# Kernel tuning notes

Hardware: AMD Instinct MI355X
Metric: run time of the kernel (lower is better)

The kernel has to match this reference:

```python
import jax, jax.numpy as jnp
import numpy as np

NUM_BRANCHES = 3
NUM_LAYERS = 4
HIDDEN = 256
IN_DIM = 128
NUM_GRAPHS = 256
NUM_CLASSES = 10
TOPK_RATIO = 0.5
GATE_INIT = 0.8


def matrix_neighbors(branch, layer, num_branches):
    nbrs = []
    if layer > 0:
        nbrs.append((branch, layer - 1))
    for other in (branch - 1, branch + 1):
        if 0 <= other < num_branches:
            nbrs.append((other, layer))
    if layer > 0:
        for other in (branch - 1, branch + 1):
            if 0 <= other < num_branches:
                nbrs.append((other, layer - 1))
    return nbrs


def topk_mask(t, ratio):
    d = t.shape[-1]
    k = max(1, min(d, int(np.ceil(d * ratio))))
    if k >= d:
        return jnp.ones_like(t)
    _, idx = jax.lax.top_k(jnp.abs(t), k)
    rows = jnp.arange(t.shape[0])[:, None]
    return jnp.zeros_like(t).at[rows, idx].set(1.0)


def setup_inputs():
    key = jax.random.key(0)
    ks = jax.random.split(key, 10)
    n, e = 50000, 800000
    x = jax.random.normal(ks[0], (n, IN_DIM), dtype=jnp.float32)
    edge_index = jax.random.randint(ks[1], (2, e), 0, n)
    batch = jnp.sort(jax.random.randint(ks[2], (n,), 0, NUM_GRAPHS))
    s = 0.05
    Win = jax.random.normal(ks[3], (NUM_BRANCHES, IN_DIM, HIDDEN), dtype=jnp.float32) * s
    b_in = jnp.zeros((NUM_BRANCHES, HIDDEN), dtype=jnp.float32)
    Whid = jax.random.normal(ks[4], (NUM_LAYERS - 1, NUM_BRANCHES, HIDDEN, HIDDEN), dtype=jnp.float32) * s
    bhid = jnp.zeros((NUM_LAYERS - 1, NUM_BRANCHES, HIDDEN), dtype=jnp.float32)
    gate_logit = jnp.asarray(np.log(GATE_INIT / (1.0 - GATE_INIT)), dtype=jnp.float32)
    Wc = jax.random.normal(ks[5], (HIDDEN, NUM_CLASSES), dtype=jnp.float32) * s
    bc = jnp.zeros((NUM_CLASSES,), dtype=jnp.float32)
    return {"x": x, "edge_index": edge_index, "batch": batch, "Win": Win,
            "b_in": b_in, "Whid": Whid, "bhid": bhid, "gate_logit": gate_logit,
            "Wc": Wc, "bc": bc}


def _forward(x, edge_index, batch, Win, b_in, Whid, bhid, gate_logit, Wc, bc):
    n = x.shape[0]
    loops = jnp.arange(n)
    row = jnp.concatenate([edge_index[0], loops])  # source
    col = jnp.concatenate([edge_index[1], loops])  # target
    deg = jax.ops.segment_sum(jnp.ones_like(col, dtype=x.dtype), col, num_segments=n)
    dinv = jnp.where(deg > 0, jax.lax.rsqrt(deg), 0.0)
    norm = dinv[row] * dinv[col]  # [E+N]

    def gcn(h, W, b):
        hw = h @ W  # [n, H]
        agg = jax.ops.segment_sum(hw[row] * norm[:, None], col, num_segments=n)
        return agg + b

    gate = jax.nn.sigmoid(gate_logit)
    states = [x for _ in range(NUM_BRANCHES)]
    for layer in range(NUM_LAYERS):
        props = []
        for b in range(NUM_BRANCHES):
            if layer == 0:
                p = gcn(states[b], Win[b], b_in[b])
            else:
                p = gcn(states[b], Whid[layer - 1, b], bhid[layer - 1, b])
            props.append(jax.nn.relu(p))
        new_states = []
        for b in range(NUM_BRANCHES):
            fused = props[b]
            nbrs = matrix_neighbors(b, layer, NUM_BRANCHES)
            if nbrs:
                rs = jnp.zeros_like(fused)
                for (sb, sl) in nbrs:
                    src = props[sb] if sl == layer else states[sb]
                    rs = rs + src * topk_mask(src, TOPK_RATIO)
                fused = fused + gate * rs
            new_states.append(jax.nn.relu(fused))  # dropout is identity in eval
        states = new_states

    counts = jax.ops.segment_sum(jnp.ones((n,), dtype=x.dtype), batch, num_segments=NUM_GRAPHS)
    denom = jnp.maximum(counts, 1.0)[:, None]
    embs = [jax.ops.segment_sum(s, batch, num_segments=NUM_GRAPHS) / denom for s in states]
    final = jnp.mean(jnp.stack(embs, axis=0), axis=0)  # [G, H]
    logits = final @ Wc + bc
    return logits, final


def reference(x, edge_index, batch, Win, b_in, Whid, bhid, gate_logit, Wc, bc):
    return _forward(x, edge_index, batch, Win, b_in, Whid, bhid, gate_logit, Wc, bc)
```

## Files before the change

kernel.cpp:

```cpp
#include <hip/hip_runtime.h>
#include <hip/hip_fp16.h>

#define NB 3
#define HIDDEN 256
#define INDIM 128
#define NGRAPH 256
#define NCLS 10
#define NMAX 50048
#define EMAX 800000

typedef unsigned short u16;
typedef unsigned long long ull;
typedef _Float16 f16_t;
typedef f16_t f16x8 __attribute__((ext_vector_type(8)));
typedef float f32x4 __attribute__((ext_vector_type(4)));

__device__ __align__(16) u16   g_states[(size_t)NMAX * NB * HIDDEN];
__device__ __align__(16) u16   g_props [(size_t)NMAX * NB * HIDDEN];
__device__ __align__(16) u16   g_agg3 [(size_t)NMAX * NB * HIDDEN];
__device__ __align__(16) u16   g_xh    [(size_t)NMAX * INDIM];
__device__ __align__(16) u16   g_whin [(size_t)NB * INDIM * HIDDEN];
__device__ __align__(16) u16   g_whid [(size_t)9 * HIDDEN * HIDDEN];
__device__ float g_fin   [NGRAPH * HIDDEN];
__device__ float g_dinv  [NMAX];
__device__ float g_ewts  [EMAX];
__device__ int   g_rowptr[NMAX + 1];
__device__ int   g_cidx  [EMAX];
__device__ int   g_cnt   [NMAX];
__device__ int   g_bsum  [64];
__device__ int   g_gs    [NGRAPH];
__device__ int   g_gc    [NGRAPH];

union HU { u16 u; __half h; };
__device__ __forceinline__ float h2f(u16 v) { HU x; x.u = v; return __half2float(x.h); }
__device__ __forceinline__ u16 f2h(float f) { HU x; x.h = __float2half_rn(f); return x.u; }
__device__ __forceinline__ float relu_f(float x) { return x > 0.f ? x : 0.f; }

__device__ __forceinline__ void fma8(float* acc, uint4 v, float w) {
    unsigned uu[4] = {v.x, v.y, v.z, v.w};
    #pragma unroll
    for (int q = 0; q < 4; ++q) {
        HU lo, hi; lo.u = (u16)(uu[q] & 0xFFFFu); hi.u = (u16)(uu[q] >> 16);
        acc[q * 2 + 0] += w * __half2float(lo.h);
        acc[q * 2 + 1] += w * __half2float(hi.h);
    }
}

__global__ void zero_cnt_k(int n) {
    int i = blockIdx.x * 256 + threadIdx.x;
    if (i < n) g_cnt[i] = 0;
}
__global__ void zero_gk() {
    int i = threadIdx.x;
    g_gs[i] = 0; g_gc[i] = 0;
}
__global__ void cvt_xh_k(const float* __restrict__ x, int cnt4) {
    int i = blockIdx.x * 256 + threadIdx.x;
    if (i >= cnt4) return;
    float4 v = ((const float4*)x)[i];
    ushort4 o; o.x = f2h(v.x); o.y = f2h(v.y); o.z = f2h(v.z); o.w = f2h(v.w);
    ((ushort4*)g_xh)[i] = o;
}
__global__ void cvt_wt_k(const float* __restrict__ src, int which, int K) {
    __shared__ u16 tile[32][33];
    int k0 = blockIdx.x * 32, c0 = blockIdx.y * 32, b = blockIdx.z;
    int t = threadIdx.x;
    int tc = t & 31, tk = t >> 5;
    const float* S = src + (size_t)b * K * 256;
    #pragma unroll
    for (int q = 0; q < 4; ++q) {
        int kk = tk * 4 + q;
        tile[kk][tc] = f2h(S[(size_t)(k0 + kk) * 256 + c0 + tc]);
    }
    __syncthreads();
    u16* D = (which ? g_whid : g_whin) + (size_t)b * K * 256;
    int kx = t & 31, cg = t >> 5;
    #pragma unroll
    for (int q = 0; q < 4; ++q) {
        int c = c0 + cg * 4 + q;
        D[(size_t)c * K + k0 + kx] = tile[kx][cg * 4 + q];
    }
}

__global__ void count_edges_k(const int* __restrict__ col, int E) {
    int i = blockIdx.x * 256 + threadIdx.x;
    if (i < E) atomicAdd(&g_cnt[col[i]], 1);
}
__global__ void dinv_k(int n) {
    int i = blockIdx.x * 256 + threadIdx.x;
    if (i < n) g_dinv[i] = rsqrtf((float)(g_cnt[i] + 1));
}
__global__ __launch_bounds__(1024) void scan1_k(int n) {
    __shared__ int sm[1024];
    int blk = blockIdx.x, t = threadIdx.x;
    int i = blk * 1024 + t;
    int v = (i < n) ? g_cnt[i] : 0;
    sm[t] = v;
    __syncthreads();
    for (int off = 1; off < 1024; off <<= 1) {
        int u = (t >= off) ? sm[t - off] : 0;
        __syncthreads();
        sm[t] += u;
        __syncthreads();
    }
    if (i < n) g_rowptr[i + 1] = sm[t];
    if (t == 1023) g_bsum[blk] = sm[t];
    if (blk == 0 && t == 0) g_rowptr[0] = 0;
}
__global__ void scan2_k(int nblk) {
    int t = threadIdx.x;
    int v = (t < nblk) ? g_bsum[t] : 0;
    #pragma unroll
    for (int off = 1; off < 64; off <<= 1) {
        int u = __shfl_up(v, off);
        if (t >= off) v += u;
    }
    if (t < nblk) g_bsum[t] = v;
}
__global__ void scan3_k(int n) {
    int i = blockIdx.x * 256 + threadIdx.x;
    if (i >= n) return;
    int blk = i >> 10;
    if (blk > 0) g_rowptr[i + 1] += g_bsum[blk - 1];
}
__global__ void fill_csr_k(const int* __restrict__ row, const int* __restrict__ col, int E) {
    int i = blockIdx.x * 256 + threadIdx.x;
    if (i >= E) return;
    int r = row[i], c = col[i];
    int pos = g_rowptr[c] + atomicAdd(&g_cnt[c], 1);
    g_cidx[pos] = r;
    g_ewts[pos] = g_dinv[r] * g_dinv[c];
}

__global__ __launch_bounds__(256) void agg256x3_k(int n) {
    int node = blockIdx.x * 4 + (threadIdx.x >> 6);
    if (node >= n) return;
    int lane = threadIdx.x & 63;
    int half = lane >> 5;
    int li   = lane & 31;
    const uint4* Sv = (const uint4*)g_states;
    float acc0[8] = {0,0,0,0,0,0,0,0}, acc1[8] = {0,0,0,0,0,0,0,0}, acc2[8] = {0,0,0,0,0,0,0,0};
    int e0 = g_rowptr[node], deg = g_rowptr[node + 1] - e0;
    int m = deg + 1;
    int j = half;
    if (half == 0) {
        float di = g_dinv[node];
        float w0 = di * di;
        size_t base = (size_t)node * 96 + li;
        fma8(acc0, Sv[base], w0);
        fma8(acc1, Sv[base + 32], w0);
        fma8(acc2, Sv[base + 64], w0);
        j = 2;
    }
    #pragma unroll 2
    for (; j < m; j += 2) {
        int s = g_cidx[e0 + j - 1];
        float w = g_ewts[e0 + j - 1];
        size_t base = (size_t)s * 96 + li;
        uint4 v0 = Sv[base], v1 = Sv[base + 32], v2 = Sv[base + 64];
        fma8(acc0, v0, w); fma8(acc1, v1, w); fma8(acc2, v2, w);
    }
    #pragma unroll
    for (int q = 0; q < 8; ++q) {
        acc0[q] += __shfl_xor(acc0[q], 32);
        acc1[q] += __shfl_xor(acc1[q], 32);
        acc2[q] += __shfl_xor(acc2[q], 32);
    }
    if (half == 0) {
        uint4* Av = (uint4*)g_agg3;
        size_t base = (size_t)node * 96 + li;
        uint4 o;
        unsigned* ou = (unsigned*)&o;
        #pragma unroll
        for (int q = 0; q < 4; ++q) ou[q] = (unsigned)f2h(acc0[q*2]) | ((unsigned)f2h(acc0[q*2+1]) << 16);
        Av[base] = o;
        #pragma unroll
        for (int q = 0; q < 4; ++q) ou[q] = (unsigned)f2h(acc1[q*2]) | ((unsigned)f2h(acc1[q*2+1]) << 16);
        Av[base + 32] = o;
        #pragma unroll
        for (int q = 0; q < 4; ++q) ou[q] = (unsigned)f2h(acc2[q*2]) | ((unsigned)f2h(acc2[q*2+1]) << 16);
        Av[base + 64] = o;
    }
}

__global__ __launch_bounds__(256) void agg128_k(int n) {
    int node = blockIdx.x * 4 + (threadIdx.x >> 6);
    if (node >= n) return;
    int lane = threadIdx.x & 63;
    int grp = lane >> 4;
    int li  = lane & 15;
    const uint4* Xv = (const uint4*)g_xh;
    float acc[8] = {0,0,0,0,0,0,0,0};
    int e0 = g_rowptr[node], deg = g_rowptr[node + 1] - e0;
    int m = deg + 1;
    int j = grp;
    if (grp == 0) {
        float di = g_dinv[node];
        fma8(acc, Xv[(size_t)node * 16 + li], di * di);
        j = 4;
    }
    #pragma unroll 2
    for (; j < m; j += 4) {
        int s = g_cidx[e0 + j - 1];
        float w = g_ewts[e0 + j - 1];
        fma8(acc, Xv[(size_t)s * 16 + li], w);
    }
    #pragma unroll
    for (int q = 0; q < 8; ++q) {
        acc[q] += __shfl_xor(acc[q], 16);
        acc[q] += __shfl_xor(acc[q], 32);
    }
    if (grp == 0) {
        uint4 o; unsigned* ou = (unsigned*)&o;
        #pragma unroll
        for (int q = 0; q < 4; ++q) ou[q] = (unsigned)f2h(acc[q*2]) | ((unsigned)f2h(acc[q*2+1]) << 16);
        ((uint4*)g_agg3)[(size_t)node * 16 + li] = o;
    }
}

template<int K>
__global__ __launch_bounds__(256) void gemm_mfma_k(int wsel, int rowStride, int brMul,
        const float* __restrict__ bias0, int n) {
    int br = blockIdx.y;
    const f16_t* A  = (const f16_t*)g_agg3 + (size_t)br * brMul;
    const f16_t* Wt = (wsel < 0) ? (const f16_t*)g_whin + (size_t)br * K * 256
                                 : (const f16_t*)g_whid + (size_t)(wsel + br) * K * 256;
    const float* bias = bias0 + (size_t)br * 256;
    u16* C = g_props + (size_t)br * 256;
    int t = threadIdx.x, l = t & 63, w = t >> 6;
    int row0 = blockIdx.x * 64;
    int c0 = w * 64;
    int mrow = l & 15;
    int kg = (l >> 4) * 8;
    f32x4 acc[4][4];
    #pragma unroll
    for (int rt = 0; rt < 4; ++rt)
        #pragma unroll
        for (int ct = 0; ct < 4; ++ct) acc[rt][ct] = (f32x4){0.f, 0.f, 0.f, 0.f};

    for (int k0 = 0; k0 < K; k0 += 32) {
        f16x8 af[4], bf[4];
        #pragma unroll
        for (int rt = 0; rt < 4; ++rt) {
            int r = row0 + rt * 16 + mrow;
            af[rt] = *(const f16x8*)(A + (size_t)r * rowStride + k0 + kg);
        }
        #pragma unroll
        for (int ct = 0; ct < 4; ++ct) {
            int c = c0 + ct * 16 + mrow;
            bf[ct] = *(const f16x8*)(Wt + (size_t)c * K + k0 + kg);
        }
        #pragma unroll
        for (int rt = 0; rt < 4; ++rt)
            #pragma unroll
            for (int ct = 0; ct < 4; ++ct)
                acc[rt][ct] = __builtin_amdgcn_mfma_f32_16x16x32_f16(af[rt], bf[ct], acc[rt][ct], 0, 0, 0);
    }
    int rb = (l >> 4) * 4;
    #pragma unroll
    for (int ct = 0; ct < 4; ++ct) {
        int c = c0 + ct * 16 + mrow;
        float bv = bias[c];
        #pragma unroll
        for (int rt = 0; rt < 4; ++rt) {
            #pragma unroll
            for (int q = 0; q < 4; ++q) {
                int r = row0 + rt * 16 + rb + q;
                if (r < n) C[(size_t)r * 768 + c] = f2h(relu_f(acc[rt][ct][q] + bv));
            }
        }
    }
}

template<int CNT>
__device__ __forceinline__ void topk_multi(const ushort4* hu, const float4* v, float4* out) {
    int lane = threadIdx.x & 63;
    unsigned lo[CNT], hi[CNT]; int cge[CNT];
    #pragma unroll
    for (int s = 0; s < CNT; ++s) {
        unsigned mx = max(max((unsigned)hu[s].x, (unsigned)hu[s].y),
                          max((unsigned)hu[s].z, (unsigned)hu[s].w));
        #pragma unroll
        for (int off = 32; off >= 1; off >>= 1)
            mx = max(mx, (unsigned)__shfl_xor((int)mx, off));
        lo[s] = 0; hi[s] = mx; cge[s] = 256;
    }
    for (int it = 0; it < 15; ++it) {
        #pragma unroll
        for (int s = 0; s < CNT; ++s) {
            if (cge[s] == 128 || lo[s] >= hi[s]) continue;
            unsigned mid = (lo[s] + hi[s] + 1) >> 1;
            int c = __popcll(__ballot(hu[s].x >= mid)) + __popcll(__ballot(hu[s].y >= mid))
                  + __popcll(__ballot(hu[s].z >= mid)) + __popcll(__ballot(hu[s].w >= mid));
            if (c >= 128) { lo[s] = mid; cge[s] = c; } else hi[s] = mid - 1;
        }
    }
    #pragma unroll
    for (int s = 0; s < CNT; ++s) {
        unsigned thr = lo[s];
        unsigned a0 = hu[s].x, a1 = hu[s].y, a2 = hu[s].z, a3 = hu[s].w;
        float4 r;
        if (cge[s] == 128) {
            r.x = (a0 >= thr) ? v[s].x : 0.f;
            r.y = (a1 >= thr) ? v[s].y : 0.f;
            r.z = (a2 >= thr) ? v[s].z : 0.f;
            r.w = (a3 >= thr) ? v[s].w : 0.f;
        } else {
            ull b0 = __ballot(a0 == thr), b1 = __ballot(a1 == thr);
            ull b2 = __ballot(a2 == thr), b3 = __ballot(a3 == thr);
            int cgt = __popcll(__ballot(a0 > thr)) + __popcll(__ballot(a1 > thr))
                    + __popcll(__ballot(a2 > thr)) + __popcll(__ballot(a3 > thr));
            int need = 128 - cgt;
            ull below = (lane == 0) ? 0ull : (~0ull >> (64 - lane));
            int base = __popcll(b0 & below) + __popcll(b1 & below)
                     + __popcll(b2 & below) + __popcll(b3 & below);
            int o0 = (int)((b0 >> lane) & 1), o1 = (int)((b1 >> lane) & 1), o2 = (int)((b2 >> lane) & 1);
            int p0 = base, p1 = base + o0, p2 = p1 + o1, p3 = p2 + o2;
            r.x = (a0 > thr || (a0 == thr && p0 < need)) ? v[s].x : 0.f;
            r.y = (a1 > thr || (a1 == thr && p1 < need)) ? v[s].y : 0.f;
            r.z = (a2 > thr || (a2 == thr && p2 < need)) ? v[s].z : 0.f;
            r.w = (a3 > thr || (a3 == thr && p3 < need)) ? v[s].w : 0.f;
        }
        out[s] = r;
    }
}

__device__ __forceinline__ float4 dec4(ushort4 h) {
    float4 r; r.x = h2f(h.x); r.y = h2f(h.y); r.z = h2f(h.z); r.w = h2f(h.w);
    return r;
}
__device__ __forceinline__ void st4h(u16* p, size_t off, float4 v) {
    ushort4 o; o.x = f2h(v.x); o.y = f2h(v.y); o.z = f2h(v.z); o.w = f2h(v.w);
    ((ushort4*)p)[off] = o;
}

__global__ __launch_bounds__(256) void fuse0_k(const float* __restrict__ gate_logit, int n) {
    int node = blockIdx.x * 4 + (threadIdx.x >> 6);
    if (node >= n) return;
    int lane = threadIdx.x & 63;
    size_t base4 = (size_t)node * 192 + lane;
    float g = 1.f / (1.f + expf(-gate_logit[0]));
    const ushort4* P = (const ushort4*)g_props;
    ushort4 hu[3]; float4 v[3], m[3];
    hu[0] = P[base4]; hu[1] = P[base4 + 64]; hu[2] = P[base4 + 128];
    v[0] = dec4(hu[0]); v[1] = dec4(hu[1]); v[2] = dec4(hu[2]);
    topk_multi<3>(hu, v, m);
    float4 o0, o1, o2;
    o0.x = relu_f(v[0].x + g * m[1].x); o0.y = relu_f(v[0].y + g * m[1].y);
    o0.z = relu_f(v[0].z + g * m[1].z); o0.w = relu_f(v[0].w + g * m[1].w);
    o1.x = relu_f(v[1].x + g * (m[0].x + m[2].x)); o1.y = relu_f(v[1].y + g * (m[0].y + m[2].y));
    o1.z = relu_f(v[1].z + g * (m[0].z + m[2].z)); o1.w = relu_f(v[1].w + g * (m[0].w + m[2].w));
    o2.x = relu_f(v[2].x + g * m[1].x); o2.y = relu_f(v[2].y + g * m[1].y);
    o2.z = relu_f(v[2].z + g * m[1].z); o2.w = relu_f(v[2].w + g * m[1].w);
    st4h(g_states, base4, o0); st4h(g_states, base4 + 64, o1); st4h(g_states, base4 + 128, o2);
}

__global__ __launch_bounds__(256) void fuse_k(const float* __restrict__ gate_logit, int n) {
    int node = blockIdx.x * 4 + (threadIdx.x >> 6);
    if (node >= n) return;
    int lane = threadIdx.x & 63;
    size_t base4 = (size_t)node * 192 + lane;
    float g = 1.f / (1.f + expf(-gate_logit[0]));
    const ushort4* P = (const ushort4*)g_props;
    const ushort4* S = (const ushort4*)g_states;
    ushort4 hu[6]; float4 v[6], m[6];
    hu[0] = P[base4]; hu[1] = P[base4 + 64]; hu[2] = P[base4 + 128];
    hu[3] = S[base4]; hu[4] = S[base4 + 64]; hu[5] = S[base4 + 128];
    #pragma unroll
    for (int s = 0; s < 6; ++s) v[s] = dec4(hu[s]);
    topk_multi<6>(hu, v, m);
    float4 o0, o1, o2;
    o0.x = relu_f(v[0].x + g * (m[3].x + m[1].x + m[4].x));
    o0.y = relu_f(v[0].y + g * (m[3].y + m[1].y + m[4].y));
    o0.z = relu_f(v[0].z + g * (m[3].z + m[1].z + m[4].z));
    o0.w = relu_f(v[0].w + g * (m[3].w + m[1].w + m[4].w));
    o1.x = relu_f(v[1].x + g * (m[4].x + m[0].x + m[3].x + m[2].x + m[5].x));
    o1.y = relu_f(v[1].y + g * (m[4].y + m[0].y + m[3].y + m[2].y + m[5].y));
    o1.z = relu_f(v[1].z + g * (m[4].z + m[0].z + m[3].z + m[2].z + m[5].z));
    o1.w = relu_f(v[1].w + g * (m[4].w + m[0].w + m[3].w + m[2].w + m[5].w));
    o2.x = relu_f(v[2].x + g * (m[5].x + m[1].x + m[4].x));
    o2.y = relu_f(v[2].y + g * (m[5].y + m[1].y + m[4].y));
    o2.z = relu_f(v[2].z + g * (m[5].z + m[1].z + m[4].z));
    o2.w = relu_f(v[2].w + g * (m[5].w + m[1].w + m[4].w));
    st4h(g_states, base4, o0); st4h(g_states, base4 + 64, o1); st4h(g_states, base4 + 128, o2);
}

__global__ void gbounds_k(const int* __restrict__ batch, int n) {
    int i = blockIdx.x * 256 + threadIdx.x;
    if (i >= n) return;
    int g = batch[i];
    atomicAdd(&g_gc[g], 1);
    if (i == 0 || batch[i - 1] != g) g_gs[g] = i;
}

__global__ __launch_bounds__(256) void greduce_k(float* __restrict__ outfin, int n) {
    __shared__ float sums[768];
    int g = blockIdx.x, t = threadIdx.x;
    int st = g_gs[g], c = g_gc[g];
    if (t < 192) {
        const ushort4* S = (const ushort4*)g_states;
        float a0 = 0.f, a1 = 0.f, a2 = 0.f, a3 = 0.f;
        for (int i = st; i < st + c; ++i) {
            ushort4 v = S[(size_t)i * 192 + t];
            a0 += h2f(v.x); a1 += h2f(v.y); a2 += h2f(v.z); a3 += h2f(v.w);
        }
        sums[t * 4 + 0] = a0; sums[t * 4 + 1] = a1;
        sums[t * 4 + 2] = a2; sums[t * 4 + 3] = a3;
    }
    __syncthreads();
    float r = (sums[t] + sums[256 + t] + sums[512 + t]) / (3.0f * (float)(c > 0 ? c : 1));
    g_fin[g * 256 + t] = r;
    outfin[(size_t)g * 256 + t] = r;
}

__global__ void logits_k(const float* __restrict__ Wc, const float* __restrict__ bc,
                         float* __restrict__ out) {
    int idx = blockIdx.x * 256 + threadIdx.x;
    if (idx >= NGRAPH * NCLS) return;
    int g = idx / NCLS, c = idx % NCLS;
    float s = bc[c];
    for (int k = 0; k < 256; ++k) s += g_fin[g * 256 + k] * Wc[k * NCLS + c];
    out[idx] = s;
}

extern "C" void kernel_launch(void* const* d_in, const int* in_sizes, int n_in,
                              void* d_out, int out_size, void* d_ws, size_t ws_size,
                              hipStream_t stream) {
    const float* x       = (const float*)d_in[0];
    const int*   eidx    = (const int*)d_in[1];
    const int*   batch   = (const int*)d_in[2];
    const float* Win     = (const float*)d_in[3];
    const float* b_in    = (const float*)d_in[4];
    const float* Whid    = (const float*)d_in[5];
    const float* bhid    = (const float*)d_in[6];
    const float* gate_l  = (const float*)d_in[7];
    const float* Wc      = (const float*)d_in[8];
    const float* bc      = (const float*)d_in[9];
    float* out = (float*)d_out;

    const int n = in_sizes[0] / INDIM;
    const int E = in_sizes[1] / 2;
    if (n > NMAX || E > EMAX) return;
    const int* erow = eidx;
    const int* ecol = eidx + E;

    float* outfin = out + NGRAPH * NCLS;

    const int TB = 256;
    dim3 b256(TB);
    int nblkN = (n + TB - 1) / TB;
    int eblk  = (E + TB - 1) / TB;
    int nblk4 = (n + 3) / 4;
    int sblk  = (n + 1023) / 1024;
    dim3 ggrid((n + 63) / 64, NB);
    dim3 wgin(INDIM / 32, HIDDEN / 32, NB);
    dim3 wghid(HIDDEN / 32, HIDDEN / 32, 9);

    zero_cnt_k<<<nblkN, b256, 0, stream>>>(n);
    cvt_xh_k<<<(n * INDIM / 4 + TB - 1) / TB, b256, 0, stream>>>(x, n * INDIM / 4);
    cvt_wt_k<<<wgin, b256, 0, stream>>>(Win, 0, INDIM);
    cvt_wt_k<<<wghid, b256, 0, stream>>>(Whid, 1, HIDDEN);
    count_edges_k<<<eblk, b256, 0, stream>>>(ecol, E);
    dinv_k<<<nblkN, b256, 0, stream>>>(n);
    scan1_k<<<sblk, 1024, 0, stream>>>(n);
    scan2_k<<<1, 64, 0, stream>>>(sblk);
    scan3_k<<<nblkN, b256, 0, stream>>>(n);
    zero_cnt_k<<<nblkN, b256, 0, stream>>>(n);
    fill_csr_k<<<eblk, b256, 0, stream>>>(erow, ecol, E);

    agg128_k<<<nblk4, b256, 0, stream>>>(n);
    gemm_mfma_k<INDIM><<<ggrid, b256, 0, stream>>>(-1, INDIM, 0, b_in, n);
    fuse0_k<<<nblk4, b256, 0, stream>>>(gate_l, n);

    for (int l = 1; l < 4; ++l) {
        agg256x3_k<<<nblk4, b256, 0, stream>>>(n);
        gemm_mfma_k<HIDDEN><<<ggrid, b256, 0, stream>>>((l - 1) * NB, NB * HIDDEN, HIDDEN,
                bhid + (size_t)(l - 1) * NB * HIDDEN, n);
        fuse_k<<<nblk4, b256, 0, stream>>>(gate_l, n);
    }

    zero_gk<<<1, 256, 0, stream>>>();
    gbounds_k<<<nblkN, b256, 0, stream>>>(batch, n);
    greduce_k<<<NGRAPH, b256, 0, stream>>>(outfin, n);
    logits_k<<<(NGRAPH * NCLS + TB - 1) / TB, b256, 0, stream>>>(Wc, bc, out);
}
```

Measured before the change: 1.698 ms.

## Fuse per-layer GEMM with top-k gated fusion via shared-memory staging

Merges the MFMA GEMM and the top-k fuse kernel into one kernel. Each block computes all three branches for 32 nodes, stages the relu'd results in LDS, then runs the top-k mixing and writes the states directly. This removes the g_props global round trip and one launch per layer. In exchange the row tile is halved to 32, so weights are reloaded more often per output row, and the large LDS footprint may lower occupancy.

New measurement: 1.937 ms. +14.1%, slower.

```diff
diff --git a/kernel.cpp b/kernel.cpp
--- a/kernel.cpp
+++ b/kernel.cpp
@@ -16,7 +16,6 @@
 typedef float f32x4 __attribute__((ext_vector_type(4)));
 
 __device__ __align__(16) u16   g_states[(size_t)NMAX * NB * HIDDEN];
-__device__ __align__(16) u16   g_props [(size_t)NMAX * NB * HIDDEN];
 __device__ __align__(16) u16   g_agg3 [(size_t)NMAX * NB * HIDDEN];
 __device__ __align__(16) u16   g_xh    [(size_t)NMAX * INDIM];
 __device__ __align__(16) u16   g_whin [(size_t)NB * INDIM * HIDDEN];
@@ -215,60 +214,6 @@
         #pragma unroll
         for (int q = 0; q < 4; ++q) ou[q] = (unsigned)f2h(acc[q*2]) | ((unsigned)f2h(acc[q*2+1]) << 16);
         ((uint4*)g_agg3)[(size_t)node * 16 + li] = o;
-    }
-}
-
-template<int K>
-__global__ __launch_bounds__(256) void gemm_mfma_k(int wsel, int rowStride, int brMul,
-        const float* __restrict__ bias0, int n) {
-    int br = blockIdx.y;
-    const f16_t* A  = (const f16_t*)g_agg3 + (size_t)br * brMul;
-    const f16_t* Wt = (wsel < 0) ? (const f16_t*)g_whin + (size_t)br * K * 256
-                                 : (const f16_t*)g_whid + (size_t)(wsel + br) * K * 256;
-    const float* bias = bias0 + (size_t)br * 256;
-    u16* C = g_props + (size_t)br * 256;
-    int t = threadIdx.x, l = t & 63, w = t >> 6;
-    int row0 = blockIdx.x * 64;
-    int c0 = w * 64;
-    int mrow = l & 15;
-    int kg = (l >> 4) * 8;
-    f32x4 acc[4][4];
-    #pragma unroll
-    for (int rt = 0; rt < 4; ++rt)
-        #pragma unroll
-        for (int ct = 0; ct < 4; ++ct) acc[rt][ct] = (f32x4){0.f, 0.f, 0.f, 0.f};
-
-    for (int k0 = 0; k0 < K; k0 += 32) {
-        f16x8 af[4], bf[4];
-        #pragma unroll
-        for (int rt = 0; rt < 4; ++rt) {
-            int r = row0 + rt * 16 + mrow;
-            af[rt] = *(const f16x8*)(A + (size_t)r * rowStride + k0 + kg);
-        }
-        #pragma unroll
-        for (int ct = 0; ct < 4; ++ct) {
-            int c = c0 + ct * 16 + mrow;
-            bf[ct] = *(const f16x8*)(Wt + (size_t)c * K + k0 + kg);
-        }
-        #pragma unroll
-        for (int rt = 0; rt < 4; ++rt)
-            #pragma unroll
-            for (int ct = 0; ct < 4; ++ct)
-                acc[rt][ct] = __builtin_amdgcn_mfma_f32_16x16x32_f16(af[rt], bf[ct], acc[rt][ct], 0, 0, 0);
-    }
-    int rb = (l >> 4) * 4;
-    #pragma unroll
-    for (int ct = 0; ct < 4; ++ct) {
-        int c = c0 + ct * 16 + mrow;
-        float bv = bias[c];
-        #pragma unroll
-        for (int rt = 0; rt < 4; ++rt) {
-            #pragma unroll
-            for (int q = 0; q < 4; ++q) {
-                int r = row0 + rt * 16 + rb + q;
-                if (r < n) C[(size_t)r * 768 + c] = f2h(relu_f(acc[rt][ct][q] + bv));
-            }
-        }
     }
 }
 
@@ -334,55 +279,103 @@
     ((ushort4*)p)[off] = o;
 }
 
-__global__ __launch_bounds__(256) void fuse0_k(const float* __restrict__ gate_logit, int n) {
-    int node = blockIdx.x * 4 + (threadIdx.x >> 6);
-    if (node >= n) return;
-    int lane = threadIdx.x & 63;
-    size_t base4 = (size_t)node * 192 + lane;
+#define LDSW 776
+template<int K, bool L0>
+__global__ __launch_bounds__(256) void gemm_fuse_k(int wsel, int rowStride, int brMul,
+        const float* __restrict__ bias0, const float* __restrict__ gate_logit, int n) {
+    __shared__ u16 lds_p[32 * LDSW];
+    int t = threadIdx.x, l = t & 63, w = t >> 6;
+    int row0 = blockIdx.x * 32;
+    int mrow = l & 15;
+    int kg = (l >> 4) * 8;
+    int rb = (l >> 4) * 4;
+
+    for (int br = 0; br < NB; ++br) {
+        const f16_t* A  = (const f16_t*)g_agg3 + (size_t)br * brMul;
+        const f16_t* Wt = (wsel < 0) ? (const f16_t*)g_whin + (size_t)br * K * 256
+                                     : (const f16_t*)g_whid + (size_t)(wsel + br) * K * 256;
+        const float* bias = bias0 + (size_t)br * 256;
+        f32x4 acc[2][4];
+        #pragma unroll
+        for (int rt = 0; rt < 2; ++rt)
+            #pragma unroll
+            for (int ct = 0; ct < 4; ++ct) acc[rt][ct] = (f32x4){0.f, 0.f, 0.f, 0.f};
+        for (int k0 = 0; k0 < K; k0 += 32) {
+            f16x8 af[2], bf[4];
+            #pragma unroll
+            for (int rt = 0; rt < 2; ++rt) {
+                int r = row0 + rt * 16 + mrow;
+                af[rt] = *(const f16x8*)(A + (size_t)r * rowStride + k0 + kg);
+            }
+            #pragma unroll
+            for (int ct = 0; ct < 4; ++ct) {
+                int c = w * 64 + ct * 16 + mrow;
+                bf[ct] = *(const f16x8*)(Wt + (size_t)c * K + k0 + kg);
+            }
+            #pragma unroll
+            for (int rt = 0; rt < 2; ++rt)
+                #pragma unroll
+                for (int ct = 0; ct < 4; ++ct)
+                    acc[rt][ct] = __builtin_amdgcn_mfma_f32_16x16x32_f16(af[rt], bf[ct], acc[rt][ct], 0, 0, 0);
+        }
+        #pragma unroll
+        for (int ct = 0; ct < 4; ++ct) {
+            int c = w * 64 + ct * 16 + mrow;
+            float bv = bias[c];
+            #pragma unroll
+            for (int rt = 0; rt < 2; ++rt) {
+                #pragma unroll
+                for (int q = 0; q < 4; ++q) {
+                    int ndl = rt * 16 + rb + q;
+                    lds_p[ndl * LDSW + br * 256 + c] = f2h(relu_f(acc[rt][ct][q] + bv));
+                }
+            }
+        }
+    }
+    __syncthreads();
+
     float g = 1.f / (1.f + expf(-gate_logit[0]));
-    const ushort4* P = (const ushort4*)g_props;
-    ushort4 hu[3]; float4 v[3], m[3];
-    hu[0] = P[base4]; hu[1] = P[base4 + 64]; hu[2] = P[base4 + 128];
-    v[0] = dec4(hu[0]); v[1] = dec4(hu[1]); v[2] = dec4(hu[2]);
-    topk_multi<3>(hu, v, m);
-    float4 o0, o1, o2;
-    o0.x = relu_f(v[0].x + g * m[1].x); o0.y = relu_f(v[0].y + g * m[1].y);
-    o0.z = relu_f(v[0].z + g * m[1].z); o0.w = relu_f(v[0].w + g * m[1].w);
-    o1.x = relu_f(v[1].x + g * (m[0].x + m[2].x)); o1.y = relu_f(v[1].y + g * (m[0].y + m[2].y));
-    o1.z = relu_f(v[1].z + g * (m[0].z + m[2].z)); o1.w = relu_f(v[1].w + g * (m[0].w + m[2].w));
-    o2.x = relu_f(v[2].x + g * m[1].x); o2.y = relu_f(v[2].y + g * m[1].y);
-    o2.z = relu_f(v[2].z + g * m[1].z); o2.w = relu_f(v[2].w + g * m[1].w);
-    st4h(g_states, base4, o0); st4h(g_states, base4 + 64, o1); st4h(g_states, base4 + 128, o2);
-}
-
-__global__ __launch_bounds__(256) void fuse_k(const float* __restrict__ gate_logit, int n) {
-    int node = blockIdx.x * 4 + (threadIdx.x >> 6);
-    if (node >= n) return;
-    int lane = threadIdx.x & 63;
-    size_t base4 = (size_t)node * 192 + lane;
-    float g = 1.f / (1.f + expf(-gate_logit[0]));
-    const ushort4* P = (const ushort4*)g_props;
-    const ushort4* S = (const ushort4*)g_states;
-    ushort4 hu[6]; float4 v[6], m[6];
-    hu[0] = P[base4]; hu[1] = P[base4 + 64]; hu[2] = P[base4 + 128];
-    hu[3] = S[base4]; hu[4] = S[base4 + 64]; hu[5] = S[base4 + 128];
-    #pragma unroll
-    for (int s = 0; s < 6; ++s) v[s] = dec4(hu[s]);
-    topk_multi<6>(hu, v, m);
-    float4 o0, o1, o2;
-    o0.x = relu_f(v[0].x + g * (m[3].x + m[1].x + m[4].x));
-    o0.y = relu_f(v[0].y + g * (m[3].y + m[1].y + m[4].y));
-    o0.z = relu_f(v[0].z + g * (m[3].z + m[1].z + m[4].z));
-    o0.w = relu_f(v[0].w + g * (m[3].w + m[1].w + m[4].w));
-    o1.x = relu_f(v[1].x + g * (m[4].x + m[0].x + m[3].x + m[2].x + m[5].x));
-    o1.y = relu_f(v[1].y + g * (m[4].y + m[0].y + m[3].y + m[2].y + m[5].y));
-    o1.z = relu_f(v[1].z + g * (m[4].z + m[0].z + m[3].z + m[2].z + m[5].z));
-    o1.w = relu_f(v[1].w + g * (m[4].w + m[0].w + m[3].w + m[2].w + m[5].w));
-    o2.x = relu_f(v[2].x + g * (m[5].x + m[1].x + m[4].x));
-    o2.y = relu_f(v[2].y + g * (m[5].y + m[1].y + m[4].y));
-    o2.z = relu_f(v[2].z + g * (m[5].z + m[1].z + m[4].z));
-    o2.w = relu_f(v[2].w + g * (m[5].w + m[1].w + m[4].w));
-    st4h(g_states, base4, o0); st4h(g_states, base4 + 64, o1); st4h(g_states, base4 + 128, o2);
+    for (int i = 0; i < 8; ++i) {
+        int ndl = w * 8 + i;
+        int node = row0 + ndl;
+        if (node >= n) break;
+        const u16* LP = lds_p + ndl * LDSW;
+        size_t base4 = (size_t)node * 192 + l;
+        ushort4 hu[L0 ? 3 : 6]; float4 v[L0 ? 3 : 6], m[L0 ? 3 : 6];
+        hu[0] = ((const ushort4*)LP)[l];
+        hu[1] = ((const ushort4*)(LP + 256))[l];
+        hu[2] = ((const ushort4*)(LP + 512))[l];
+        if constexpr (!L0) {
+            const ushort4* S = (const ushort4*)g_states;
+            hu[3] = S[base4]; hu[4] = S[base4 + 64]; hu[5] = S[base4 + 128];
+        }
+        #pragma unroll
+        for (int s = 0; s < (L0 ? 3 : 6); ++s) v[s] = dec4(hu[s]);
+        topk_multi<L0 ? 3 : 6>(hu, v, m);
+        float4 o0, o1, o2;
+        if constexpr (L0) {
+            o0.x = relu_f(v[0].x + g * m[1].x); o0.y = relu_f(v[0].y + g * m[1].y);
+            o0.z = relu_f(v[0].z + g * m[1].z); o0.w = relu_f(v[0].w + g * m[1].w);
+            o1.x = relu_f(v[1].x + g * (m[0].x + m[2].x)); o1.y = relu_f(v[1].y + g * (m[0].y + m[2].y));
+            o1.z = relu_f(v[1].z + g * (m[0].z + m[2].z)); o1.w = relu_f(v[1].w + g * (m[0].w + m[2].w));
+            o2.x = relu_f(v[2].x + g * m[1].x); o2.y = relu_f(v[2].y + g * m[1].y);
+            o2.z = relu_f(v[2].z + g * m[1].z); o2.w = relu_f(v[2].w + g * m[1].w);
+        } else {
+            o0.x = relu_f(v[0].x + g * (m[3].x + m[1].x + m[4].x));
+            o0.y = relu_f(v[0].y + g * (m[3].y + m[1].y + m[4].y));
+            o0.z = relu_f(v[0].z + g * (m[3].z + m[1].z + m[4].z));
+            o0.w = relu_f(v[0].w + g * (m[3].w + m[1].w + m[4].w));
+            o1.x = relu_f(v[1].x + g * (m[4].x + m[0].x + m[3].x + m[2].x + m[5].x));
+            o1.y = relu_f(v[1].y + g * (m[4].y + m[0].y + m[3].y + m[2].y + m[5].y));
+            o1.z = relu_f(v[1].z + g * (m[4].z + m[0].z + m[3].z + m[2].z + m[5].z));
+            o1.w = relu_f(v[1].w + g * (m[4].w + m[0].w + m[3].w + m[2].w + m[5].w));
+            o2.x = relu_f(v[2].x + g * (m[5].x + m[1].x + m[4].x));
+            o2.y = relu_f(v[2].y + g * (m[5].y + m[1].y + m[4].y));
+            o2.z = relu_f(v[2].z + g * (m[5].z + m[1].z + m[4].z));
+            o2.w = relu_f(v[2].w + g * (m[5].w + m[1].w + m[4].w));
+        }
+        st4h(g_states, base4, o0); st4h(g_states, base4 + 64, o1); st4h(g_states, base4 + 128, o2);
+    }
 }
 
 __global__ void gbounds_k(const int* __restrict__ batch, int n) {
@@ -452,7 +445,7 @@
     int eblk  = (E + TB - 1) / TB;
     int nblk4 = (n + 3) / 4;
     int sblk  = (n + 1023) / 1024;
-    dim3 ggrid((n + 63) / 64, NB);
+    int gfblk = (n + 31) / 32;
     dim3 wgin(INDIM / 32, HIDDEN / 32, NB);
     dim3 wghid(HIDDEN / 32, HIDDEN / 32, 9);
 
@@ -469,14 +462,12 @@
     fill_csr_k<<<eblk, b256, 0, stream>>>(erow, ecol, E);
 
     agg128_k<<<nblk4, b256, 0, stream>>>(n);
-    gemm_mfma_k<INDIM><<<ggrid, b256, 0, stream>>>(-1, INDIM, 0, b_in, n);
-    fuse0_k<<<nblk4, b256, 0, stream>>>(gate_l, n);
+    gemm_fuse_k<INDIM, true><<<gfblk, b256, 0, stream>>>(-1, INDIM, 0, b_in, gate_l, n);
 
     for (int l = 1; l < 4; ++l) {
         agg256x3_k<<<nblk4, b256, 0, stream>>>(n);
-        gemm_mfma_k<HIDDEN><<<ggrid, b256, 0, stream>>>((l - 1) * NB, NB * HIDDEN, HIDDEN,
-                bhid + (size_t)(l - 1) * NB * HIDDEN, n);
-        fuse_k<<<nblk4, b256, 0, stream>>>(gate_l, n);
+        gemm_fuse_k<HIDDEN, false><<<gfblk, b256, 0, stream>>>((l - 1) * NB, NB * HIDDEN, HIDDEN,
+                bhid + (size_t)(l - 1) * NB * HIDDEN, gate_l, n);
     }
 
     zero_gk<<<1, 256, 0, stream>>>();
```
